# Performance work log

Hardware: AMD Instinct MI355X
Metric: run time of the kernel (lower is better)

## Reference

```python
import jax, jax.numpy as jnp
import numpy as np

NUM_CLASSES = 80
CONF_THRESH = 0.05
NMS_THRESH = 0.6
TOPK = 1000
LEVEL_HWS = [40000, 10000, 2500, 640, 160]
CLASS_OFFSET = 2.0  # > max box coordinate so different classes never overlap (class-aware NMS)


def setup_inputs() -> dict:
    key = jax.random.key(0)
    inp = {}
    for i, hw in enumerate(LEVEL_HWS):
        k1, k2, k3, key = jax.random.split(key, 4)
        inp[f"cls_p{i + 3}"] = jax.random.normal(k1, (1, hw, NUM_CLASSES), jnp.float32)
        inp[f"ctn_p{i + 3}"] = jax.random.normal(k2, (1, hw, 1), jnp.float32)
        inp[f"box_p{i + 3}"] = jax.random.uniform(k3, (1, hw, 4), jnp.float32)
    inp["img_size"] = 1600
    return inp


def _level_select(cls_p, ctn_p, box_p):
    # cls_p: [1, HW, C], ctn_p: [1, HW, 1], box_p: [1, HW, 4]
    cls_p, ctn_p, box_p = cls_p[0], ctn_p[0], box_p[0]
    k = min(TOPK, box_p.shape[0])  # matches min(self.topk, box_pred_i.size(0))
    scores = jnp.sqrt(jax.nn.sigmoid(cls_p) * jax.nn.sigmoid(ctn_p)).reshape(-1)  # [HW*C]
    topk_scores, topk_idxs = jax.lax.top_k(scores, k)  # descending, == sort+slice
    valid = topk_scores > CONF_THRESH  # mask instead of dynamic filter (jit-friendly)
    labels = topk_idxs % NUM_CLASSES
    anchor_idxs = topk_idxs // NUM_CLASSES
    return topk_scores * valid, labels, box_p[anchor_idxs], valid


def _pairwise_iou(boxes):
    # boxes: [N, 4] xyxy
    x1, y1, x2, y2 = boxes[:, 0], boxes[:, 1], boxes[:, 2], boxes[:, 3]
    area = jnp.maximum(x2 - x1, 0.0) * jnp.maximum(y2 - y1, 0.0)
    ix1 = jnp.maximum(x1[:, None], x1[None, :])
    iy1 = jnp.maximum(y1[:, None], y1[None, :])
    ix2 = jnp.minimum(x2[:, None], x2[None, :])
    iy2 = jnp.minimum(y2[:, None], y2[None, :])
    inter = jnp.maximum(ix2 - ix1, 0.0) * jnp.maximum(iy2 - iy1, 0.0)
    union = area[:, None] + area[None, :] - inter
    return inter / jnp.maximum(union, 1e-9)


def _greedy_nms(scores, boxes, valid, thresh):
    # exact greedy NMS over a fixed-size candidate set; returns keep mask [N]
    n = scores.shape[0]
    order = jnp.argsort(-scores)
    iou = _pairwise_iou(boxes[order])  # [N, N]
    idx = jnp.arange(n)

    def body(i, keep):
        sup = (iou[i] > thresh) & keep[i] & (idx > i)
        return keep & (~sup)

    keep_o = jax.lax.fori_loop(0, n, body, valid[order])
    return jnp.zeros(n, dtype=bool).at[order].set(keep_o)


def reference(cls_p3, ctn_p3, box_p3, cls_p4, ctn_p4, box_p4,
              cls_p5, ctn_p5, box_p5, cls_p6, ctn_p6, box_p6,
              cls_p7, ctn_p7, box_p7, img_size):
    levels = [(cls_p3, ctn_p3, box_p3), (cls_p4, ctn_p4, box_p4),
              (cls_p5, ctn_p5, box_p5), (cls_p6, ctn_p6, box_p6),
              (cls_p7, ctn_p7, box_p7)]
    parts = [_level_select(c, t, b) for (c, t, b) in levels]
    scores = jnp.concatenate([p[0] for p in parts])   # [3800]
    labels = jnp.concatenate([p[1] for p in parts])   # [3800] int
    bboxes = jnp.concatenate([p[2] for p in parts])   # [3800, 4]
    valid = jnp.concatenate([p[3] for p in parts])    # [3800] bool
    # class-aware multiclass NMS via coordinate offset per class
    boxes_off = bboxes + (labels.astype(bboxes.dtype) * CLASS_OFFSET)[:, None]
    keep = _greedy_nms(jax.lax.stop_gradient(scores),
                       jax.lax.stop_gradient(boxes_off), valid, NMS_THRESH)
    # normalize to [0,1] by image size (square image: W == H == img_size)
    bboxes_n = jnp.clip(bboxes / jnp.float32(img_size), 0.0, 1.0)
    return scores * keep, labels, bboxes_n, keep
```

## Files before the change

### kernel.cpp

```cpp
#include <hip/hip_runtime.h>
#include <math.h>

#pragma clang fp contract(off)

#define NCLS 80
#define NTOT 3800
#define CAND_CAP 4096
#define NMS_CAP 1024
#define BIN_LO 0x3F000000u
#define NB 1024
#define BSHIFT 13
#define QPB 1024
#define NBLK 1044
#define PBUF_CAP 320

__constant__ int d_BSQ[6]  = {0, 782, 978, 1027, 1040, 1044};
__constant__ int d_QL[5]   = {800000, 200000, 50000, 12800, 3200};
__constant__ int d_EL[5]   = {3200000, 800000, 200000, 51200, 12800};
__constant__ float d_PREHI[5] = {0.86f, 0.82f, 0.78f, 0.74f, 0.74f};
__constant__ int d_SEGCAP[5]  = {64, 96, 192, 320, 320};
__constant__ int d_SEGBASE[5] = {0, 50048, 68864, 78272, 82432};
__constant__ int d_KL[5] = {1000,1000,1000,640,160};
__constant__ int d_OB[5] = {0,1000,2000,3000,3640};

struct Params {
  const float *cls0,*cls1,*cls2,*cls3,*cls4;
  const float *ctn0,*ctn1,*ctn2,*ctn3,*ctn4;
  const float *box0,*box1,*box2,*box3,*box4;
  const int* img;
  unsigned short* blockhist;
  unsigned* tot;
  unsigned* blkcnt;
  unsigned long long* pre;
  unsigned* slot_bits;
  unsigned* slot_label;
  float* slot_box;
  float* out;
};

__device__ __forceinline__ float fast_sig(float x) {
  return 1.0f / (1.0f + __expf(-x));
}
__device__ __forceinline__ float fast_score(float c, float t) {
  return sqrtf(fast_sig(c) * fast_sig(t));
}

__device__ __forceinline__ float sigmoid_ref(float x) {
  float e = (float)exp(-(double)x);
  return 1.0f / (1.0f + e);
}
__device__ __forceinline__ float score_ref(float c, float t) {
  return sqrtf(sigmoid_ref(c) * sigmoid_ref(t));
}

__device__ __forceinline__ float iou_ref(float ax1,float ay1,float ax2,float ay2,
                                         float bx1,float by1,float bx2,float by2) {
  float areaA = fmaxf(ax2-ax1,0.0f) * fmaxf(ay2-ay1,0.0f);
  float areaB = fmaxf(bx2-bx1,0.0f) * fmaxf(by2-by1,0.0f);
  float ix1 = fmaxf(ax1,bx1), iy1 = fmaxf(ay1,by1);
  float ix2 = fminf(ax2,bx2), iy2 = fminf(ay2,by2);
  float inter = fmaxf(ix2-ix1,0.0f) * fmaxf(iy2-iy1,0.0f);
  float uni = areaA + areaB - inter;
  return inter / fmaxf(uni, 1e-9f);
}

__device__ __forceinline__ const float* cls_of(const Params& p, int l) {
  return (l==0)?p.cls0:(l==1)?p.cls1:(l==2)?p.cls2:(l==3)?p.cls3:p.cls4;
}
__device__ __forceinline__ const float* ctn_of(const Params& p, int l) {
  return (l==0)?p.ctn0:(l==1)?p.ctn1:(l==2)?p.ctn2:(l==3)?p.ctn3:p.ctn4;
}
__device__ __forceinline__ const float* box_of(const Params& p, int l) {
  return (l==0)?p.box0:(l==1)?p.box1:(l==2)?p.box2:(l==3)?p.box3:p.box4;
}

__global__ __launch_bounds__(256) void k_score(Params p) {
  int b = blockIdx.x, tid = threadIdx.x;
  __shared__ unsigned h[NB];
  __shared__ unsigned long long pbuf[PBUF_CAP];
  __shared__ unsigned pcnt;
  for (int i = tid; i < NB; i += 256) h[i] = 0u;
  if (tid == 0) pcnt = 0u;
  __syncthreads();
  int l = 0;
  while (b >= d_BSQ[l+1]) ++l;
  int cb = b - d_BSQ[l];
  int q0 = cb * QPB;
  int nq = d_QL[l] - q0; if (nq > QPB) nq = QPB;
  const float* cls = cls_of(p, l);
  const float* ctn = ctn_of(p, l);
  float prehi = d_PREHI[l];
  for (int i = tid; i < nq; i += 256) {
    int q = q0 + i;
    float4 c4 = ((const float4*)cls)[q];
    float st = fast_sig(ctn[q / 20]);
    float s[4];
    s[0] = sqrtf(fast_sig(c4.x) * st);
    s[1] = sqrtf(fast_sig(c4.y) * st);
    s[2] = sqrtf(fast_sig(c4.z) * st);
    s[3] = sqrtf(fast_sig(c4.w) * st);
    #pragma unroll
    for (int j = 0; j < 4; ++j) {
      unsigned bits = __float_as_uint(s[j]);
      if (bits >= BIN_LO) atomicAdd(&h[(bits - BIN_LO) >> BSHIFT], 1u);
      if (s[j] >= prehi) {
        unsigned pos = atomicAdd(&pcnt, 1u);
        if (pos < PBUF_CAP)
          pbuf[pos] = ((unsigned long long)bits << 32)
                    | (unsigned long long)(0xFFFFFFFFu - (unsigned)(4*q + j));
      }
    }
  }
  __syncthreads();
  unsigned short* hout = p.blockhist + (size_t)b * NB;
  for (int i = tid; i < NB; i += 256) hout[i] = (unsigned short)h[i];
  int cap = d_SEGCAP[l];
  unsigned n = pcnt;
  if (tid == 0) p.blkcnt[b] = n;
  unsigned nw = n < (unsigned)cap ? n : (unsigned)cap;
  unsigned long long* seg = p.pre + d_SEGBASE[l] + (size_t)cb * cap;
  for (unsigned i = tid; i < nw; i += 256) seg[i] = pbuf[i];
}

__global__ __launch_bounds__(256) void k_reduce(Params p) {
  int l = blockIdx.x >> 4, c = blockIdx.x & 15, tid = threadIdx.x;
  int b0 = d_BSQ[l], rows = d_BSQ[l+1] - b0;
  int bin = c*64 + (tid & 63);
  int rlane = tid >> 6;
  const unsigned short* bh = p.blockhist + (size_t)b0 * NB + bin;
  unsigned a0=0,a1=0,a2=0,a3=0;
  int r = rlane;
  for (; r + 12 < rows; r += 16) {
    a0 += bh[(size_t)r * NB];
    a1 += bh[(size_t)(r+4) * NB];
    a2 += bh[(size_t)(r+8) * NB];
    a3 += bh[(size_t)(r+12) * NB];
  }
  for (; r < rows; r += 4) a0 += bh[(size_t)r * NB];
  __shared__ unsigned red[256];
  red[tid] = a0+a1+a2+a3;
  __syncthreads();
  if (tid < 64)
    p.tot[l*NB + c*64 + tid] = red[tid] + red[tid+64] + red[tid+128] + red[tid+192];
}

__global__ __launch_bounds__(1024) void k_sort_out(Params p) {
  int l = blockIdx.x, tid = threadIdx.x;
  __shared__ unsigned long long cand[CAND_CAP];
  __shared__ unsigned tot[NB];
  __shared__ unsigned csum[256];
  __shared__ unsigned ccnt;
  __shared__ int bad;
  __shared__ unsigned thr_s;
  if (tid == 0) { ccnt = 0u; bad = 0; }
  if (tid < NB) tot[tid] = p.tot[l*NB + tid];
  __syncthreads();
  if (tid < 256) {
    unsigned s = 0;
    for (int j = 0; j < 4; ++j) s += tot[tid*4 + j];
    csum[tid] = s;
  }
  __syncthreads();
  if (tid == 0) {
    unsigned k = (unsigned)d_KL[l];
    unsigned cum = 0; int chunk = 255;
    for (; chunk > 0; --chunk) {
      if (cum + csum[chunk] >= k) break;
      cum += csum[chunk];
    }
    int binf = 0; int found = 0;
    unsigned c2 = cum;
    for (int i = 3; i >= 0; --i) {
      int bin = chunk*4 + i;
      c2 += tot[bin];
      if (c2 >= k) { binf = bin; found = 1; break; }
    }
    unsigned t = BIN_LO;
    if (found && binf > 0) t = BIN_LO + ((unsigned)(binf - 1) << BSHIFT);
    thr_s = t;
  }
  __syncthreads();
  unsigned thr = thr_s;
  int b0 = d_BSQ[l], nseg = d_BSQ[l+1] - b0, cap = d_SEGCAP[l];
  for (int s = tid; s < nseg; s += 1024)
    if (p.blkcnt[b0 + s] > (unsigned)cap) bad = 1;
  __syncthreads();
  const float* cls = cls_of(p, l);
  const float* ctn = ctn_of(p, l);
  bool fastok = (!bad) && (thr >= __float_as_uint(d_PREHI[l]));
  if (fastok) {
    int total = nseg * cap;
    const unsigned long long* base = p.pre + d_SEGBASE[l];
    for (int i = tid; i < total; i += 1024) {
      int s = i / cap, j = i - s*cap;
      if (j < (int)p.blkcnt[b0 + s]) {
        unsigned long long kk = base[(size_t)s*cap + j];
        if ((unsigned)(kk >> 32) >= thr) {
          unsigned pos = atomicAdd(&ccnt, 1u);
          if (pos < CAND_CAP) cand[pos] = kk;
        }
      }
    }
  } else {
    int ne = d_EL[l];
    for (int e = tid; e < ne; e += 1024) {
      float s = fast_score(cls[e], ctn[e / NCLS]);
      unsigned bits = __float_as_uint(s);
      if (bits >= thr) {
        unsigned pos = atomicAdd(&ccnt, 1u);
        if (pos < CAND_CAP)
          cand[pos] = ((unsigned long long)bits << 32)
                    | (unsigned long long)(0xFFFFFFFFu - (unsigned)e);
      }
    }
  }
  __syncthreads();
  int m = (ccnt < CAND_CAP) ? (int)ccnt : CAND_CAP;
  for (int i = tid; i < m; i += 1024) {
    unsigned fi = 0xFFFFFFFFu - (unsigned)(cand[i] & 0xFFFFFFFFu);
    float ex = score_ref(cls[fi], ctn[fi / NCLS]);
    cand[i] = ((unsigned long long)__float_as_uint(ex) << 32)
            | (unsigned long long)(0xFFFFFFFFu - fi);
  }
  __syncthreads();
  int kL = d_KL[l], obase = d_OB[l];
  float img = (float)(*p.img);
  const float* box = box_of(p, l);
  for (int i = tid; i < m; i += 1024) {
    unsigned long long mine = cand[i];
    int rank = 0;
    for (int j = 0; j < m; ++j) rank += (cand[j] > mine) ? 1 : 0;
    if (rank < kL) {
      int g = obase + rank;
      unsigned bits = (unsigned)(mine >> 32);
      unsigned fi = 0xFFFFFFFFu - (unsigned)(mine & 0xFFFFFFFFu);
      unsigned lab = fi % NCLS;
      unsigned a = fi / NCLS;
      p.out[NTOT + g] = (float)lab;
      for (int j = 0; j < 4; ++j) {
        float bv = box[a*4 + j];
        float nb = bv / img;
        nb = fminf(fmaxf(nb, 0.0f), 1.0f);
        p.out[2*NTOT + g*4 + j] = nb;
        p.slot_box[g*4 + j] = bv;
      }
      p.slot_bits[g] = bits;
      p.slot_label[g] = lab;
    }
  }
  for (int r = m + tid; r < kL; r += 1024) {
    int g = obase + r;
    p.out[NTOT + g] = 0.0f;
    for (int j = 0; j < 4; ++j) { p.out[2*NTOT + g*4 + j] = 0.0f; p.slot_box[g*4+j] = 0.0f; }
    p.slot_bits[g] = 0u; p.slot_label[g] = 0u;
  }
}

__global__ __launch_bounds__(64) void k_nms(Params p) {
  int c = blockIdx.x, tid = threadIdx.x;
  __shared__ unsigned mcnt;
  __shared__ unsigned long long key[NMS_CAP];
  __shared__ unsigned long long skey[NMS_CAP];
  __shared__ float bx[NMS_CAP*4];
  __shared__ int keep[NMS_CAP];
  if (tid == 0) mcnt = 0u;
  __syncthreads();
  for (int g = tid; g < NTOT; g += 64) {
    if (p.slot_label[g] == (unsigned)c) {
      unsigned pos = atomicAdd(&mcnt, 1u);
      if (pos < NMS_CAP)
        key[pos] = ((unsigned long long)p.slot_bits[g] << 32)
                 | (unsigned long long)(0xFFFFFFFFu - (unsigned)g);
    }
  }
  __syncthreads();
  int m = (mcnt < NMS_CAP) ? (int)mcnt : NMS_CAP;
  if (m == 0) return;
  for (int i = tid; i < m; i += 64) {
    unsigned long long mine = key[i];
    int rank = 0;
    for (int j = 0; j < m; ++j) rank += (key[j] > mine) ? 1 : 0;
    skey[rank] = mine;
  }
  __syncthreads();
  float off = 2.0f * (float)c;
  for (int j = tid; j < m; j += 64) {
    unsigned long long kk = skey[j];
    unsigned g = 0xFFFFFFFFu - (unsigned)(kk & 0xFFFFFFFFu);
    for (int q = 0; q < 4; ++q) bx[j*4+q] = p.slot_box[g*4+q] + off;
    float s = __uint_as_float((unsigned)(kk >> 32));
    keep[j] = (s > 0.05f) ? 1 : 0;
  }
  __syncthreads();
  for (int i = 0; i + 1 < m; ++i) {
    if (keep[i]) {
      float ax1 = bx[i*4+0], ay1 = bx[i*4+1], ax2 = bx[i*4+2], ay2 = bx[i*4+3];
      for (int j = i + 1 + tid; j < m; j += 64) {
        if (keep[j]) {
          if (iou_ref(ax1,ay1,ax2,ay2, bx[j*4+0],bx[j*4+1],bx[j*4+2],bx[j*4+3]) > 0.6f)
            keep[j] = 0;
        }
      }
    }
    __syncthreads();
  }
  for (int j = tid; j < m; j += 64) {
    unsigned long long kk = skey[j];
    unsigned g = 0xFFFFFFFFu - (unsigned)(kk & 0xFFFFFFFFu);
    float s = __uint_as_float((unsigned)(kk >> 32));
    int kp = keep[j];
    p.out[g] = kp ? s : 0.0f;
    p.out[6*NTOT + g] = kp ? 1.0f : 0.0f;
  }
}

extern "C" void kernel_launch(void* const* d_in, const int* in_sizes, int n_in,
                              void* d_out, int out_size, void* d_ws, size_t ws_size,
                              hipStream_t stream) {
  Params p;
  p.cls0 = (const float*)d_in[0];  p.ctn0 = (const float*)d_in[1];  p.box0 = (const float*)d_in[2];
  p.cls1 = (const float*)d_in[3];  p.ctn1 = (const float*)d_in[4];  p.box1 = (const float*)d_in[5];
  p.cls2 = (const float*)d_in[6];  p.ctn2 = (const float*)d_in[7];  p.box2 = (const float*)d_in[8];
  p.cls3 = (const float*)d_in[9];  p.ctn3 = (const float*)d_in[10]; p.box3 = (const float*)d_in[11];
  p.cls4 = (const float*)d_in[12]; p.ctn4 = (const float*)d_in[13]; p.box4 = (const float*)d_in[14];
  p.img  = (const int*)d_in[15];

  char* w = (char*)d_ws;
  p.pre = (unsigned long long*)w;   w += (size_t)83712 * 8;
  p.blockhist = (unsigned short*)w; w += (size_t)NBLK*NB*2;
  p.tot  = (unsigned*)w;            w += (size_t)5*NB*4;
  p.blkcnt = (unsigned*)w;          w += (size_t)NBLK*4 + 64;
  p.slot_bits  = (unsigned*)w;      w += NTOT*4;
  p.slot_label = (unsigned*)w;      w += NTOT*4;
  p.slot_box   = (float*)w;         w += NTOT*16;
  p.out = (float*)d_out;

  hipLaunchKernelGGL(k_score,    dim3(NBLK), dim3(256),  0, stream, p);
  hipLaunchKernelGGL(k_reduce,   dim3(80),   dim3(256),  0, stream, p);
  hipLaunchKernelGGL(k_sort_out, dim3(5),    dim3(1024), 0, stream, p);
  hipLaunchKernelGGL(k_nms,      dim3(80),   dim3(64),   0, stream, p);
}
```

Before: 230.7 us.

## Split rank-sort into separate kernel spread across many blocks

The per-level candidate rank sort, which used to run in five 1024-thread blocks, now runs in its own kernel with 320 blocks of 64 threads. Candidate keys pass through global workspace. Each block copies its level's keys into shared memory and ranks a 64-element slice with an 8-way unrolled compare loop. Box gathers and output stores use float4. The goal is to spread the O(m^2) ranking over more CUs, at the cost of an extra launch and a global round trip for the keys.

Result: faster. 218.5 us (-5.3%).

```diff
diff --git a/kernel.cpp b/kernel.cpp
--- a/kernel.cpp
+++ b/kernel.cpp
@@ -32,6 +32,8 @@
   unsigned* tot;
   unsigned* blkcnt;
   unsigned long long* pre;
+  unsigned long long* ckey;
+  unsigned* ccount;
   unsigned* slot_bits;
   unsigned* slot_label;
   float* slot_box;
@@ -144,7 +146,7 @@
     p.tot[l*NB + c*64 + tid] = red[tid] + red[tid+64] + red[tid+128] + red[tid+192];
 }
 
-__global__ __launch_bounds__(1024) void k_sort_out(Params p) {
+__global__ __launch_bounds__(1024) void k_gather(Params p) {
   int l = blockIdx.x, tid = threadIdx.x;
   __shared__ unsigned long long cand[CAND_CAP];
   __shared__ unsigned tot[NB];
@@ -216,44 +218,63 @@
   }
   __syncthreads();
   int m = (ccnt < CAND_CAP) ? (int)ccnt : CAND_CAP;
+  unsigned long long* ck = p.ckey + (size_t)l * CAND_CAP;
   for (int i = tid; i < m; i += 1024) {
     unsigned fi = 0xFFFFFFFFu - (unsigned)(cand[i] & 0xFFFFFFFFu);
     float ex = score_ref(cls[fi], ctn[fi / NCLS]);
-    cand[i] = ((unsigned long long)__float_as_uint(ex) << 32)
-            | (unsigned long long)(0xFFFFFFFFu - fi);
-  }
-  __syncthreads();
+    ck[i] = ((unsigned long long)__float_as_uint(ex) << 32)
+          | (unsigned long long)(0xFFFFFFFFu - fi);
+  }
+  if (tid == 0) p.ccount[l] = (unsigned)m;
   int kL = d_KL[l], obase = d_OB[l];
-  float img = (float)(*p.img);
-  const float* box = box_of(p, l);
-  for (int i = tid; i < m; i += 1024) {
-    unsigned long long mine = cand[i];
-    int rank = 0;
-    for (int j = 0; j < m; ++j) rank += (cand[j] > mine) ? 1 : 0;
-    if (rank < kL) {
-      int g = obase + rank;
-      unsigned bits = (unsigned)(mine >> 32);
-      unsigned fi = 0xFFFFFFFFu - (unsigned)(mine & 0xFFFFFFFFu);
-      unsigned lab = fi % NCLS;
-      unsigned a = fi / NCLS;
-      p.out[NTOT + g] = (float)lab;
-      for (int j = 0; j < 4; ++j) {
-        float bv = box[a*4 + j];
-        float nb = bv / img;
-        nb = fminf(fmaxf(nb, 0.0f), 1.0f);
-        p.out[2*NTOT + g*4 + j] = nb;
-        p.slot_box[g*4 + j] = bv;
-      }
-      p.slot_bits[g] = bits;
-      p.slot_label[g] = lab;
-    }
-  }
   for (int r = m + tid; r < kL; r += 1024) {
     int g = obase + r;
     p.out[NTOT + g] = 0.0f;
     for (int j = 0; j < 4; ++j) { p.out[2*NTOT + g*4 + j] = 0.0f; p.slot_box[g*4+j] = 0.0f; }
     p.slot_bits[g] = 0u; p.slot_label[g] = 0u;
   }
+}
+
+__global__ __launch_bounds__(64) void k_rank(Params p) {
+  int bx = blockIdx.x;
+  int l = bx >> 6, slice = bx & 63;
+  int tid = threadIdx.x;
+  __shared__ unsigned long long key[CAND_CAP];
+  int m = (int)p.ccount[l];
+  int i0 = slice * 64;
+  if (i0 >= m) return;
+  const unsigned long long* ck = p.ckey + (size_t)l * CAND_CAP;
+  for (int j = tid; j < m; j += 64) key[j] = ck[j];
+  __syncthreads();
+  int i = i0 + tid;
+  if (i >= m) return;
+  unsigned long long mine = key[i];
+  int rank = 0;
+  int mm = m & ~7;
+  #pragma unroll 1
+  for (int j = 0; j < mm; j += 8) {
+    rank += (key[j  ] > mine) + (key[j+1] > mine) + (key[j+2] > mine) + (key[j+3] > mine)
+          + (key[j+4] > mine) + (key[j+5] > mine) + (key[j+6] > mine) + (key[j+7] > mine);
+  }
+  for (int j = mm; j < m; ++j) rank += (key[j] > mine) ? 1 : 0;
+  if (rank >= d_KL[l]) return;
+  int g = d_OB[l] + rank;
+  unsigned bits = (unsigned)(mine >> 32);
+  unsigned fi = 0xFFFFFFFFu - (unsigned)(mine & 0xFFFFFFFFu);
+  unsigned lab = fi % NCLS;
+  unsigned a = fi / NCLS;
+  float img = (float)(*p.img);
+  float4 b4 = ((const float4*)box_of(p, l))[a];
+  float4 nb;
+  nb.x = fminf(fmaxf(b4.x / img, 0.0f), 1.0f);
+  nb.y = fminf(fmaxf(b4.y / img, 0.0f), 1.0f);
+  nb.z = fminf(fmaxf(b4.z / img, 0.0f), 1.0f);
+  nb.w = fminf(fmaxf(b4.w / img, 0.0f), 1.0f);
+  p.out[NTOT + g] = (float)lab;
+  ((float4*)(p.out + 2*NTOT))[g] = nb;
+  ((float4*)p.slot_box)[g] = b4;
+  p.slot_bits[g] = bits;
+  p.slot_label[g] = lab;
 }
 
 __global__ __launch_bounds__(64) void k_nms(Params p) {
@@ -330,13 +351,16 @@
   p.blockhist = (unsigned short*)w; w += (size_t)NBLK*NB*2;
   p.tot  = (unsigned*)w;            w += (size_t)5*NB*4;
   p.blkcnt = (unsigned*)w;          w += (size_t)NBLK*4 + 64;
+  p.ckey = (unsigned long long*)w;  w += (size_t)5*CAND_CAP*8;
+  p.ccount = (unsigned*)w;          w += 32;
   p.slot_bits  = (unsigned*)w;      w += NTOT*4;
   p.slot_label = (unsigned*)w;      w += NTOT*4;
   p.slot_box   = (float*)w;         w += NTOT*16;
   p.out = (float*)d_out;
 
-  hipLaunchKernelGGL(k_score,    dim3(NBLK), dim3(256),  0, stream, p);
-  hipLaunchKernelGGL(k_reduce,   dim3(80),   dim3(256),  0, stream, p);
-  hipLaunchKernelGGL(k_sort_out, dim3(5),    dim3(1024), 0, stream, p);
-  hipLaunchKernelGGL(k_nms,      dim3(80),   dim3(64),   0, stream, p);
-}
+  hipLaunchKernelGGL(k_score,  dim3(NBLK),  dim3(256),  0, stream, p);
+  hipLaunchKernelGGL(k_reduce, dim3(80),    dim3(256),  0, stream, p);
+  hipLaunchKernelGGL(k_gather, dim3(5),     dim3(1024), 0, stream, p);
+  hipLaunchKernelGGL(k_rank,   dim3(5*64),  dim3(64),   0, stream, p);
+  hipLaunchKernelGGL(k_nms,    dim3(80),    dim3(64),   0, stream, p);
+}
```
